# Kernel tuning notes

Measured on AMD Instinct MI355X. Metric: run time of the kernel, lower is better.

The kernel has to match this reference:

```python
import jax, jax.numpy as jnp
import numpy as np

B, Q, T, C = 2, 300, 25, 256
NH, NL, NP = 8, 4, 4
DFF = 1024
HD = C // NH
SHAPES = [(128, 128), (64, 64), (32, 32), (16, 16)]  # (H_l, W_l) per level
S = sum(h * w for h, w in SHAPES)
LQ = Q * T


def setup_inputs() -> dict:
    key = jax.random.key(0)
    ks = jax.random.split(key, 16)
    rn = lambda k, shape, s=0.02: jax.random.normal(k, shape, jnp.float32) * s
    starts = np.cumsum([0] + [h * w for h, w in SHAPES[:-1]])
    return {
        "tgt_text": jax.random.normal(ks[0], (B, Q, T, C), jnp.float32),
        "query_pos_text": jax.random.normal(ks[1], (B, Q, T, C), jnp.float32),
        "reference_points": jax.random.uniform(ks[2], (B, LQ, NL, 2), jnp.float32),
        "src": jax.random.normal(ks[3], (B, S, C), jnp.float32),
        "src_spatial_shapes": jnp.array(SHAPES, jnp.int32),
        "level_start_index": jnp.array(starts, jnp.int32),
        "in_proj_w": rn(ks[4], (3 * C, C)), "in_proj_b": jnp.zeros((3 * C,), jnp.float32),
        "out_proj_w": rn(ks[5], (C, C)), "out_proj_b": jnp.zeros((C,), jnp.float32),
        "ln1_g": jnp.ones((C,), jnp.float32), "ln1_b": jnp.zeros((C,), jnp.float32),
        "samp_off_w": rn(ks[6], (NH * NL * NP * 2, C)), "samp_off_b": rn(ks[7], (NH * NL * NP * 2,), 0.5),
        "aw_w": rn(ks[8], (NH * NL * NP, C)), "aw_b": jnp.zeros((NH * NL * NP,), jnp.float32),
        "vp_w": rn(ks[9], (C, C)), "vp_b": jnp.zeros((C,), jnp.float32),
        "op_w": rn(ks[10], (C, C)), "op_b": jnp.zeros((C,), jnp.float32),
        "ln2_g": jnp.ones((C,), jnp.float32), "ln2_b": jnp.zeros((C,), jnp.float32),
        "ffn1_w": rn(ks[11], (DFF, C)), "ffn1_b": jnp.zeros((DFF,), jnp.float32),
        "ffn2_w": rn(ks[12], (C, DFF)), "ffn2_b": jnp.zeros((C,), jnp.float32),
        "ln3_g": jnp.ones((C,), jnp.float32), "ln3_b": jnp.zeros((C,), jnp.float32),
    }


def _ln(x, g, b):
    m = jnp.mean(x, axis=-1, keepdims=True)
    v = jnp.var(x, axis=-1, keepdims=True)
    return (x - m) / jnp.sqrt(v + 1e-5) * g + b


def _self_attn(tgt, pos, in_proj_w, in_proj_b, out_proj_w, out_proj_b):
    # torch nn.MultiheadAttention math: q,k carry pos, v is raw tgt
    qk = (tgt + pos).reshape(B * Q, T, C)
    x = tgt.reshape(B * Q, T, C)
    Wq, Wk, Wv = jnp.split(in_proj_w, 3, axis=0)
    bq, bk, bv = jnp.split(in_proj_b, 3, axis=0)
    heads = lambda t: t.reshape(B * Q, T, NH, HD).transpose(0, 2, 1, 3)
    q = heads(qk @ Wq.T + bq)
    k = heads(qk @ Wk.T + bk)
    v = heads(x @ Wv.T + bv)
    attn = jax.nn.softmax(jnp.einsum("bhqd,bhkd->bhqk", q, k) / jnp.sqrt(jnp.float32(HD)), axis=-1)
    o = jnp.einsum("bhqk,bhkd->bhqd", attn, v).transpose(0, 2, 1, 3).reshape(B * Q, T, C)
    return (o @ out_proj_w.T + out_proj_b).reshape(B, Q, T, C)


def _ms_deform_attn(query, reference_points, src, shapes, samp_off_w, samp_off_b, aw_w, aw_b, vp_w, vp_b, op_w, op_b):
    # query: [B, LQ, C]; src: [B, S, C]
    value = (src @ vp_w.T + vp_b).reshape(B, S, NH, HD)
    off = (query @ samp_off_w.T + samp_off_b).reshape(B, LQ, NH, NL, NP, 2)
    aw = jax.nn.softmax((query @ aw_w.T + aw_b).reshape(B, LQ, NH, NL * NP), axis=-1)
    aw = aw.reshape(B, LQ, NH, NL, NP)
    # normalizer is (W_l, H_l)
    norm = jnp.array([[w, h] for (h, w) in shapes], jnp.float32)
    loc = reference_points[:, :, None, :, None, :] + off / norm[None, None, None, :, None, :]
    starts = np.cumsum([0] + [h * w for h, w in shapes])
    accum = jnp.zeros((B, NH, LQ, HD), jnp.float32)
    for l, (Hl, Wl) in enumerate(shapes):
        vl = value[:, starts[l]:starts[l] + Hl * Wl].transpose(0, 2, 1, 3)  # [B,NH,HW,HD]
        # grid_sample align_corners=False pixel coords
        xl = (loc[:, :, :, l, :, 0] * Wl - 0.5).transpose(0, 2, 1, 3).reshape(B, NH, LQ * NP)
        yl = (loc[:, :, :, l, :, 1] * Hl - 0.5).transpose(0, 2, 1, 3).reshape(B, NH, LQ * NP)
        x0 = jnp.floor(xl); y0 = jnp.floor(yl)
        wx1 = xl - x0; wy1 = yl - y0
        x0i = x0.astype(jnp.int32); y0i = y0.astype(jnp.int32)
        samp = jnp.zeros((B, NH, LQ * NP, HD), jnp.float32)
        for dx, dy, w in ((0, 0, (1 - wx1) * (1 - wy1)), (1, 0, wx1 * (1 - wy1)),
                          (0, 1, (1 - wx1) * wy1), (1, 1, wx1 * wy1)):
            xi = x0i + dx; yi = y0i + dy
            valid = (xi >= 0) & (xi < Wl) & (yi >= 0) & (yi < Hl)
            lin = jnp.clip(yi, 0, Hl - 1) * Wl + jnp.clip(xi, 0, Wl - 1)
            g = jnp.take_along_axis(vl, lin[..., None], axis=2)  # [B,NH,LQ*NP,HD]
            samp = samp + g * (w * valid)[..., None]
        samp = samp.reshape(B, NH, LQ, NP, HD)
        awl = aw[:, :, :, l, :].transpose(0, 2, 1, 3)  # [B,NH,LQ,NP]
        accum = accum + jnp.sum(samp * awl[..., None], axis=3)
    out = accum.transpose(0, 2, 1, 3).reshape(B, LQ, C)
    return out @ op_w.T + op_b


def reference(tgt_text, query_pos_text, reference_points, src, src_spatial_shapes, level_start_index,
              in_proj_w, in_proj_b, out_proj_w, out_proj_b, ln1_g, ln1_b,
              samp_off_w, samp_off_b, aw_w, aw_b, vp_w, vp_b, op_w, op_b, ln2_g, ln2_b,
              ffn1_w, ffn1_b, ffn2_w, ffn2_b, ln3_g, ln3_b):
    shapes = [tuple(int(v) for v in row) for row in np.asarray(src_spatial_shapes)]  # static
    # --- intra-text self-attention ---
    tgt2 = _self_attn(tgt_text, query_pos_text, in_proj_w, in_proj_b, out_proj_w, out_proj_b)
    tgt = _ln(tgt_text + tgt2, ln1_g, ln1_b)
    # --- multi-scale deformable cross-attention ---
    query = (tgt + query_pos_text).reshape(B, LQ, C)
    cross = _ms_deform_attn(query, reference_points, src, shapes,
                            samp_off_w, samp_off_b, aw_w, aw_b, vp_w, vp_b, op_w, op_b)
    tgt = _ln(tgt + cross.reshape(B, Q, T, C), ln2_g, ln2_b)
    # --- FFN ---
    ffn = jax.nn.relu(tgt @ ffn1_w.T + ffn1_b) @ ffn2_w.T + ffn2_b
    return _ln(tgt + ffn, ln3_g, ln3_b)
```

## Files before the change

kernel.cpp:

```cpp
#include <hip/hip_runtime.h>
#include <cstddef>

#define B_ 2
#define Q_ 300
#define T_ 25
#define C_ 256
#define NH_ 8
#define NL_ 4
#define NP_ 4
#define HD_ 32
#define DFF_ 1024
#define LQ_ (Q_ * T_)
#define NTOK_ (B_ * LQ_)
#define S_ 21760
#define BS_ (B_ * S_)

typedef __bf16 bf16x8 __attribute__((ext_vector_type(8)));
typedef float floatx4 __attribute__((ext_vector_type(4)));
typedef unsigned short ushort_t;

__device__ __forceinline__ unsigned pack_bf16(float x, float y) {
    unsigned ux = __float_as_uint(x) + 0x8000u;
    unsigned uy = __float_as_uint(y) + 0x8000u;
    return (ux >> 16) | (uy & 0xFFFF0000u);
}
__device__ __forceinline__ ushort_t f2bf_s(float x) {
    return (ushort_t)((__float_as_uint(x) + 0x8000u) >> 16);
}
__device__ __forceinline__ float bf2f(ushort_t u) {
    return __uint_as_float((unsigned)u << 16);
}

#define WOFF_IP   0
#define WOFF_OUT  196608
#define WOFF_VP   262144
#define WOFF_SO   327680
#define WOFF_AW   393216
#define WOFF_OP   425984
#define WOFF_F1   491520
#define WOFF_F2   753664
#define WTOTAL    1015808

__global__ __launch_bounds__(256) void convw_kernel(
    const float* __restrict__ ipw, const float* __restrict__ outw,
    const float* __restrict__ vpw, const float* __restrict__ sampw,
    const float* __restrict__ aww, const float* __restrict__ opw,
    const float* __restrict__ f1w, const float* __restrict__ f2w,
    ushort_t* __restrict__ dst)
{
    long long g = ((long long)blockIdx.x * 256 + threadIdx.x) * 8;
    if (g >= WTOTAL) return;
    const float* src; long long off;
    if      (g < WOFF_OUT) { src = ipw;   off = WOFF_IP; }
    else if (g < WOFF_VP)  { src = outw;  off = WOFF_OUT; }
    else if (g < WOFF_SO)  { src = vpw;   off = WOFF_VP; }
    else if (g < WOFF_AW)  { src = sampw; off = WOFF_SO; }
    else if (g < WOFF_OP)  { src = aww;   off = WOFF_AW; }
    else if (g < WOFF_F1)  { src = opw;   off = WOFF_OP; }
    else if (g < WOFF_F2)  { src = f1w;   off = WOFF_F1; }
    else                   { src = f2w;   off = WOFF_F2; }
    const float4* s4 = (const float4*)(src + (g - off));
    float4 a = s4[0], b = s4[1];
    uint4 o;
    o.x = pack_bf16(a.x, a.y); o.y = pack_bf16(a.z, a.w);
    o.z = pack_bf16(b.x, b.y); o.w = pack_bf16(b.z, b.w);
    *(uint4*)(dst + g) = o;
}

#define GBN 128
#define GBK 64
#define LDA_S 72

template<int AMODE, int OUTMODE, int GBMT>
__global__ __launch_bounds__(256) void gemm_w(
    const void* __restrict__ Av, const float* __restrict__ A2,
    const ushort_t* __restrict__ W,
    const float* __restrict__ bias, const float* __restrict__ bias2, int N1,
    void* __restrict__ Cv, long long partStride,
    int M, int N, int K, int kChunk, int ldc, int relu)
{
    constexpr int LA = GBMT / 16;
    constexpr int LB = 8;
    constexpr int WM = GBMT / 2;
    constexpr int NI = WM / 16;

    __shared__ unsigned short SH[GBMT * LDA_S + GBN * LDA_S];
    unsigned short* Asl = SH;
    unsigned short* Bsl = SH + GBMT * LDA_S;

    const int m0 = blockIdx.x * GBMT;
    if (m0 >= M) return;
    const int n0 = blockIdx.y * GBN;
    const int z  = blockIdx.z;
    const int kbeg = z * kChunk;
    const int kend = min(K, kbeg + kChunk);

    const int t  = threadIdx.x;
    const int wid  = t >> 6;
    const int lane = t & 63;
    const int wm = (wid >> 1) * WM;
    const int wn = (wid & 1) * 64;
    const int fm = lane & 15;
    const int fq = (lane >> 4) * 8;

    const bool addA2 = (AMODE == 1) && (n0 < N1);

    floatx4 acc[NI][4];
    #pragma unroll
    for (int i = 0; i < NI; ++i)
        #pragma unroll
        for (int j = 0; j < 4; ++j)
            acc[i][j] = (floatx4){0.f, 0.f, 0.f, 0.f};

    float4 pa[LA];
    uint2  pab[LA];
    uint2  pwb[LB];
    const float* Af = (const float*)Av;
    const ushort_t* Ab = (const ushort_t*)Av;

    auto load_tiles = [&](int k0) {
        #pragma unroll
        for (int i = 0; i < LA; ++i) {
            int idx = t + 256 * i;
            int row = idx >> 4;
            int c4  = (idx & 15) * 4;
            int gm = m0 + row;
            if constexpr (AMODE == 2) {
                uint2 v = {0u, 0u};
                if (gm < M) v = *(const uint2*)(Ab + (size_t)gm * K + k0 + c4);
                pab[i] = v;
            } else {
                float4 v = make_float4(0.f, 0.f, 0.f, 0.f);
                if (gm < M) {
                    v = *(const float4*)(Af + (size_t)gm * K + k0 + c4);
                    if constexpr (AMODE == 1) {
                        if (addA2) {
                            float4 v2 = *(const float4*)(A2 + (size_t)gm * K + k0 + c4);
                            v.x += v2.x; v.y += v2.y; v.z += v2.z; v.w += v2.w;
                        }
                    }
                }
                pa[i] = v;
            }
        }
        #pragma unroll
        for (int i = 0; i < LB; ++i) {
            int idx = t + 256 * i;
            int row = idx >> 4;
            int c4  = (idx & 15) * 4;
            pwb[i] = *(const uint2*)(W + (size_t)(n0 + row) * K + k0 + c4);
        }
    };

    load_tiles(kbeg);
    for (int k0 = kbeg; k0 < kend; k0 += GBK) {
        #pragma unroll
        for (int i = 0; i < LA; ++i) {
            int idx = t + 256 * i;
            int row = idx >> 4;
            int c4  = (idx & 15) * 4;
            if constexpr (AMODE == 2) {
                *(uint2*)&Asl[row * LDA_S + c4] = pab[i];
            } else {
                uint2 p;
                p.x = pack_bf16(pa[i].x, pa[i].y);
                p.y = pack_bf16(pa[i].z, pa[i].w);
                *(uint2*)&Asl[row * LDA_S + c4] = p;
            }
        }
        #pragma unroll
        for (int i = 0; i < LB; ++i) {
            int idx = t + 256 * i;
            int row = idx >> 4;
            int c4  = (idx & 15) * 4;
            *(uint2*)&Bsl[row * LDA_S + c4] = pwb[i];
        }
        __syncthreads();
        if (k0 + GBK < kend) load_tiles(k0 + GBK);

        #pragma unroll
        for (int kk = 0; kk < 2; ++kk) {
            bf16x8 af[NI], bfr[4];
            #pragma unroll
            for (int i = 0; i < NI; ++i)
                af[i] = *(const bf16x8*)&Asl[(wm + i * 16 + fm) * LDA_S + kk * 32 + fq];
            #pragma unroll
            for (int j = 0; j < 4; ++j)
                bfr[j] = *(const bf16x8*)&Bsl[(wn + j * 16 + fm) * LDA_S + kk * 32 + fq];

            #pragma unroll
            for (int i = 0; i < NI; ++i)
                #pragma unroll
                for (int j = 0; j < 4; ++j)
                    acc[i][j] = __builtin_amdgcn_mfma_f32_16x16x32_bf16(af[i], bfr[j], acc[i][j], 0, 0, 0);
        }
        __syncthreads();
    }

    float* Cf = (float*)Cv + (long long)z * partStride;
    ushort_t* Cb = (ushort_t*)Cv;
    const int cr = (lane >> 4) * 4;
    const int cc = lane & 15;

    if constexpr (OUTMODE == 0) {
        #pragma unroll
        for (int j = 0; j < 4; ++j) {
            int gn = n0 + wn + j * 16 + cc;
            float bia = 0.f;
            if (z == 0) bia = (bias2 && gn >= N1) ? bias2[gn - N1] : bias[gn];
            #pragma unroll
            for (int i = 0; i < NI; ++i)
                #pragma unroll
                for (int r = 0; r < 4; ++r) {
                    int gm = m0 + wm + i * 16 + cr + r;
                    if (gm < M) {
                        float v = acc[i][j][r] + bia;
                        if (relu) v = fmaxf(v, 0.f);
                        Cf[(size_t)gm * ldc + gn] = v;
                    }
                }
        }
    } else {
        unsigned short* epi = SH + wid * (WM * 64);
        #pragma unroll
        for (int j = 0; j < 4; ++j) {
            int gn = n0 + wn + j * 16 + cc;
            float bia = (bias2 && gn >= N1) ? bias2[gn - N1] : bias[gn];
            #pragma unroll
            for (int i = 0; i < NI; ++i)
                #pragma unroll
                for (int r = 0; r < 4; ++r) {
                    float v = acc[i][j][r] + bia;
                    if (relu) v = fmaxf(v, 0.f);
                    epi[(i * 16 + cr + r) * 64 + j * 16 + cc] = f2bf_s(v);
                }
        }
        #pragma unroll
        for (int pass = 0; pass < WM / 8; ++pass) {
            int lr = pass * 8 + (lane >> 3);
            int gm = m0 + wm + lr;
            uint4 vv = *(const uint4*)&epi[lr * 64 + (lane & 7) * 8];
            if (gm < M) {
                if constexpr (OUTMODE == 1) {
                    *(uint4*)&Cb[(size_t)gm * ldc + n0 + wn + (lane & 7) * 8] = vv;
                } else {
                    int bb = gm >= S_;
                    int s  = gm - bb * S_;
                    int gh = n0 + wn + (lane & 7) * 8;
                    *(uint4*)&Cb[(((size_t)(bb * 8 + (gh >> 5))) * S_ + s) * 32 + (gh & 31)] = vv;
                }
            }
        }
    }
}

__global__ __launch_bounds__(64) void attn_kernel(
    const ushort_t* __restrict__ qkv,
    ushort_t* __restrict__ o)
{
    int sh = blockIdx.x;
    int s = sh >> 3, h = sh & 7;
    __shared__ float qs[T_][HD_], ks[T_][HD_], vs[T_][HD_];
    int t = threadIdx.x;

    for (int idx = t; idx < T_ * HD_; idx += 64) {
        int i = idx >> 5, d = idx & 31;
        size_t base = ((size_t)(s * T_ + i)) * 768 + h * HD_ + d;
        qs[i][d] = bf2f(qkv[base]);
        ks[i][d] = bf2f(qkv[base + 256]);
        vs[i][d] = bf2f(qkv[base + 512]);
    }
    __syncthreads();

    if (t < T_) {
        float sc[T_];
        float mx = -1e30f;
        #pragma unroll
        for (int j = 0; j < T_; ++j) {
            float dot = 0.f;
            #pragma unroll
            for (int d = 0; d < HD_; ++d) dot += qs[t][d] * ks[j][d];
            sc[j] = dot * 0.17677669529663687f;
            mx = fmaxf(mx, sc[j]);
        }
        float sum = 0.f;
        #pragma unroll
        for (int j = 0; j < T_; ++j) { sc[j] = __expf(sc[j] - mx); sum += sc[j]; }
        float inv = 1.f / sum;
        float out[HD_];
        #pragma unroll
        for (int d = 0; d < HD_; ++d) out[d] = 0.f;
        for (int j = 0; j < T_; ++j) {
            float p = sc[j] * inv;
            #pragma unroll
            for (int d = 0; d < HD_; ++d) out[d] += p * vs[j][d];
        }
        size_t ob = ((size_t)(s * T_ + t)) * C_ + h * HD_;
        #pragma unroll
        for (int d = 0; d < HD_; ++d) o[ob + d] = f2bf_s(out[d]);
    }
}

__global__ __launch_bounds__(256) void ln4_kernel(
    const float* x, const float* r,
    int nparts, long long rstride,
    const float* __restrict__ g, const float* __restrict__ b,
    float* out, const float* __restrict__ pos,
    float* qout)
{
    const int wave = threadIdx.x >> 6;
    const int lane = threadIdx.x & 63;
    const int tok = blockIdx.x * 4 + wave;
    const size_t base = (size_t)tok * C_ + lane * 4;

    float4 v = *(const float4*)(x + base);
    for (int p = 0; p < nparts; ++p) {
        float4 rv = *(const float4*)(r + base + (long long)p * rstride);
        v.x += rv.x; v.y += rv.y; v.z += rv.z; v.w += rv.w;
    }
    float s  = v.x + v.y + v.z + v.w;
    float ss = v.x * v.x + v.y * v.y + v.z * v.z + v.w * v.w;
    #pragma unroll
    for (int m = 32; m; m >>= 1) {
        s  += __shfl_xor(s, m);
        ss += __shfl_xor(ss, m);
    }
    float mean = s * (1.f / 256.f);
    float var  = ss * (1.f / 256.f) - mean * mean;
    float rstd = rsqrtf(var + 1e-5f);

    float4 gv = *(const float4*)(g + lane * 4);
    float4 bv = *(const float4*)(b + lane * 4);
    float4 y;
    y.x = (v.x - mean) * rstd * gv.x + bv.x;
    y.y = (v.y - mean) * rstd * gv.y + bv.y;
    y.z = (v.z - mean) * rstd * gv.z + bv.z;
    y.w = (v.w - mean) * rstd * gv.w + bv.w;
    *(float4*)(out + base) = y;
    if (qout) {
        float4 pv = *(const float4*)(pos + base);
        float4 q;
        q.x = y.x + pv.x; q.y = y.y + pv.y; q.z = y.z + pv.z; q.w = y.w + pv.w;
        *(float4*)(qout + base) = q;
    }
}

#define DCHUNK_ 118
__global__ __launch_bounds__(256, 4) void deform_kernel(
    const ushort_t* __restrict__ value,
    const float* __restrict__ d12,
    const float* __restrict__ refpts,
    ushort_t* __restrict__ out)
{
    const int bi    = blockIdx.x;
    const int xcd   = bi & 7;
    const int yy    = bi >> 3;
    const int combo = xcd + 8 * (yy & 1);
    const int chunk = yy >> 1;
    const int h     = combo & 7;
    const int b     = combo >> 3;

    __shared__ float tls[64][60];

    const int tid = threadIdx.x;
    const int t0  = chunk * 64;

    #pragma unroll
    for (int i = 0; i < 2; ++i) {
        int idx  = tid + 256 * i;
        int trw  = idx >> 3;
        int c4   = (idx & 7) * 4;
        int tl   = min(t0 + trw, LQ_ - 1);
        float4 v;
        v.x = __builtin_nontemporal_load(d12 + (size_t)(b * LQ_ + tl) * 384 + h * 32 + c4 + 0);
        v.y = __builtin_nontemporal_load(d12 + (size_t)(b * LQ_ + tl) * 384 + h * 32 + c4 + 1);
        v.z = __builtin_nontemporal_load(d12 + (size_t)(b * LQ_ + tl) * 384 + h * 32 + c4 + 2);
        v.w = __builtin_nontemporal_load(d12 + (size_t)(b * LQ_ + tl) * 384 + h * 32 + c4 + 3);
        *(float4*)&tls[trw][c4] = v;
    }
    {
        int trw = tid >> 2;
        int c4  = (tid & 3) * 4;
        int tl  = min(t0 + trw, LQ_ - 1);
        float4 v;
        v.x = __builtin_nontemporal_load(d12 + (size_t)(b * LQ_ + tl) * 384 + 256 + h * 16 + c4 + 0);
        v.y = __builtin_nontemporal_load(d12 + (size_t)(b * LQ_ + tl) * 384 + 256 + h * 16 + c4 + 1);
        v.z = __builtin_nontemporal_load(d12 + (size_t)(b * LQ_ + tl) * 384 + 256 + h * 16 + c4 + 2);
        v.w = __builtin_nontemporal_load(d12 + (size_t)(b * LQ_ + tl) * 384 + 256 + h * 16 + c4 + 3);
        *(float4*)&tls[trw][32 + c4] = v;
    }
    if (tid < 128) {
        int trw = tid >> 1;
        int c4  = (tid & 1) * 4;
        int tl  = min(t0 + trw, LQ_ - 1);
        float4 v;
        v.x = __builtin_nontemporal_load(refpts + (size_t)(b * LQ_ + tl) * 8 + c4 + 0);
        v.y = __builtin_nontemporal_load(refpts + (size_t)(b * LQ_ + tl) * 8 + c4 + 1);
        v.z = __builtin_nontemporal_load(refpts + (size_t)(b * LQ_ + tl) * 8 + c4 + 2);
        v.w = __builtin_nontemporal_load(refpts + (size_t)(b * LQ_ + tl) * 8 + c4 + 3);
        *(float4*)&tls[trw][48 + c4] = v;
    }
    __syncthreads();

    if (tid < 64) {
        float lg[16];
        float mx = -1e30f;
        #pragma unroll
        for (int i = 0; i < 16; ++i) { lg[i] = tls[tid][32 + i]; mx = fmaxf(mx, lg[i]); }
        float sum = 0.f;
        #pragma unroll
        for (int i = 0; i < 16; ++i) { lg[i] = __expf(lg[i] - mx); sum += lg[i]; }
        float inv = 1.f / sum;
        #pragma unroll
        for (int i = 0; i < 16; ++i) tls[tid][32 + i] = lg[i] * inv;
    }
    __syncthreads();

    const int wave = tid >> 6;
    const int lane = tid & 63;
    const int ti   = lane >> 2;
    const int d8   = (lane & 3) * 8;
    const int row  = wave * 16 + ti;

    int tl = t0 + row;
    const bool active = (tl < LQ_);
    tl = min(tl, LQ_ - 1);
    const int tok = b * LQ_ + tl;

    const int HW[4]     = {128, 64, 32, 16};
    const int starts[4] = {0, 16384, 20480, 21504};

    const ushort_t* vplane = value + (size_t)combo * ((size_t)S_ * HD_) + d8;
    const float* trow = tls[row];

    float accv[8];
    #pragma unroll
    for (int i = 0; i < 8; ++i) accv[i] = 0.f;

    #pragma unroll
    for (int l = 0; l < 4; ++l) {
        const int Hl = HW[l], Wl = HW[l];
        float rx = trow[48 + l * 2 + 0];
        float ry = trow[48 + l * 2 + 1];
        const ushort_t* vbase = vplane + (size_t)starts[l] * HD_;

        int   voff[16];
        float wgt[16];
        #pragma unroll
        for (int p = 0; p < 4; ++p) {
            float ox = trow[l * 8 + p * 2 + 0];
            float oy = trow[l * 8 + p * 2 + 1];
            float aww = trow[32 + l * 4 + p];
            float xl = rx * (float)Wl + ox - 0.5f;
            float yl = ry * (float)Hl + oy - 0.5f;
            float x0f = floorf(xl), y0f = floorf(yl);
            int x0 = (int)x0f, y0 = (int)y0f;
            float wx1 = xl - x0f, wy1 = yl - y0f;
            float wx0 = 1.f - wx1, wy0 = 1.f - wy1;
            #pragma unroll
            for (int c = 0; c < 4; ++c) {
                int dx = c & 1, dy = c >> 1;
                int xi = x0 + dx, yi = y0 + dy;
                float w = (dx ? wx1 : wx0) * (dy ? wy1 : wy0);
                bool valid = (xi >= 0) & (xi < Wl) & (yi >= 0) & (yi < Hl);
                int xc = min(max(xi, 0), Wl - 1);
                int yc = min(max(yi, 0), Hl - 1);
                voff[p * 4 + c] = yc * Wl + xc;
                wgt[p * 4 + c]  = (valid ? w : 0.f) * aww;
            }
        }
        uint4 raw[16];
        #pragma unroll
        for (int i = 0; i < 16; ++i)
            raw[i] = *(const uint4*)(vbase + (size_t)voff[i] * HD_);
        #pragma unroll
        for (int i = 0; i < 16; ++i) {
            float wc = wgt[i];
            accv[0] += __uint_as_float((raw[i].x & 0xFFFFu) << 16) * wc;
            accv[1] += __uint_as_float(raw[i].x & 0xFFFF0000u) * wc;
            accv[2] += __uint_as_float((raw[i].y & 0xFFFFu) << 16) * wc;
            accv[3] += __uint_as_float(raw[i].y & 0xFFFF0000u) * wc;
            accv[4] += __uint_as_float((raw[i].z & 0xFFFFu) << 16) * wc;
            accv[5] += __uint_as_float(raw[i].z & 0xFFFF0000u) * wc;
            accv[6] += __uint_as_float((raw[i].w & 0xFFFFu) << 16) * wc;
            accv[7] += __uint_as_float(raw[i].w & 0xFFFF0000u) * wc;
        }
    }
    if (active) {
        uint4 po;
        po.x = pack_bf16(accv[0], accv[1]);
        po.y = pack_bf16(accv[2], accv[3]);
        po.z = pack_bf16(accv[4], accv[5]);
        po.w = pack_bf16(accv[6], accv[7]);
        *(uint4*)(out + (size_t)tok * C_ + h * HD_ + d8) = po;
    }
}

extern "C" void kernel_launch(void* const* d_in, const int* in_sizes, int n_in,
                              void* d_out, int out_size, void* d_ws, size_t ws_size,
                              hipStream_t stream) {
    const float* tgt_text = (const float*)d_in[0];
    const float* pos      = (const float*)d_in[1];
    const float* refpts   = (const float*)d_in[2];
    const float* src      = (const float*)d_in[3];
    const float* in_proj_w  = (const float*)d_in[6];
    const float* in_proj_b  = (const float*)d_in[7];
    const float* out_proj_w = (const float*)d_in[8];
    const float* out_proj_b = (const float*)d_in[9];
    const float* ln1_g = (const float*)d_in[10];
    const float* ln1_b = (const float*)d_in[11];
    const float* samp_off_w = (const float*)d_in[12];
    const float* samp_off_b = (const float*)d_in[13];
    const float* aw_w = (const float*)d_in[14];
    const float* aw_b = (const float*)d_in[15];
    const float* vp_w = (const float*)d_in[16];
    const float* vp_b = (const float*)d_in[17];
    const float* op_w = (const float*)d_in[18];
    const float* op_b = (const float*)d_in[19];
    const float* ln2_g = (const float*)d_in[20];
    const float* ln2_b = (const float*)d_in[21];
    const float* ffn1_w = (const float*)d_in[22];
    const float* ffn1_b = (const float*)d_in[23];
    const float* ffn2_w = (const float*)d_in[24];
    const float* ffn2_b = (const float*)d_in[25];
    const float* ln3_g = (const float*)d_in[26];
    const float* ln3_b = (const float*)d_in[27];

    const long long NC = (long long)NTOK_ * C_;
    float* ws = (float*)d_ws;
    float* A    = ws;
    float* Bq   = ws + NC;
    float* Creg = ws + 2 * NC;
    float* D12  = Creg + (long long)NTOK_ * DFF_;
    float* E    = D12 + (long long)NTOK_ * 384;
    float* F    = E + NC;
    ushort_t* wb = (ushort_t*)(F + NC);

    ushort_t* qkv  = (ushort_t*)Creg;
    ushort_t* valt = (ushort_t*)Creg + (size_t)NTOK_ * 768;

    const int MB64P  = 240;
    const int MB128P = 120;
    const int MBV64  = BS_ / 64;

    convw_kernel<<<496, 256, 0, stream>>>(in_proj_w, out_proj_w, vp_w, samp_off_w,
                                          aw_w, op_w, ffn1_w, ffn2_w, wb);
    gemm_w<1, 1, 64><<<dim3(MB64P, 6, 1), 256, 0, stream>>>(tgt_text, pos, wb + WOFF_IP,
        in_proj_b, nullptr, 512, qkv, 0, NTOK_, 768, 256, 256, 768, 0);
    gemm_w<0, 2, 64><<<dim3(MBV64, 2, 1), 256, 0, stream>>>(src, nullptr, wb + WOFF_VP,
        vp_b, nullptr, 0, valt, 0, BS_, 256, 256, 256, 0, 0);
    attn_kernel<<<B_ * Q_ * NH_, 64, 0, stream>>>(qkv, (ushort_t*)E);
    gemm_w<2, 0, 64><<<dim3(MB64P, 2, 1), 256, 0, stream>>>(E, nullptr, wb + WOFF_OUT,
        out_proj_b, nullptr, 0, F, 0, NTOK_, 256, 256, 256, 256, 0);
    ln4_kernel<<<NTOK_ / 4, 256, 0, stream>>>(tgt_text, F, 1, 0,
                                              ln1_g, ln1_b, A, pos, Bq);
    gemm_w<0, 0, 64><<<dim3(MB64P, 3, 1), 256, 0, stream>>>(Bq, nullptr, wb + WOFF_SO,
        samp_off_b, aw_b, 256, D12, 0, NTOK_, 384, 256, 256, 384, 0);
    deform_kernel<<<8 * 2 * DCHUNK_, 256, 0, stream>>>(valt, D12, refpts, (ushort_t*)E);
    gemm_w<2, 0, 64><<<dim3(MB64P, 2, 1), 256, 0, stream>>>(E, nullptr, wb + WOFF_OP,
        op_b, nullptr, 0, F, 0, NTOK_, 256, 256, 256, 256, 0);
    ln4_kernel<<<NTOK_ / 4, 256, 0, stream>>>(A, F, 1, 0,
                                              ln2_g, ln2_b, A, nullptr, nullptr);
    gemm_w<0, 1, 128><<<dim3(MB128P, 8, 1), 256, 0, stream>>>(A, nullptr, wb + WOFF_F1,
        ffn1_b, nullptr, 0, Creg, 0, NTOK_, DFF_, 256, 256, DFF_, 1);
    gemm_w<2, 0, 128><<<dim3(MB128P, 2, 2), 256, 0, stream>>>(Creg, nullptr, wb + WOFF_F2,
        ffn2_b, nullptr, 0, E, NC, NTOK_, 256, 1024, 512, 256, 0);
    ln4_kernel<<<NTOK_ / 4, 256, 0, stream>>>(A, E, 2, NC,
                                              ln3_g, ln3_b, (float*)d_out, nullptr, nullptr);
}
```

Before: 384.2 us.

## Fuse N=256 output GEMMs with residual add and LayerNorm in one kernel

Adds a gemm_ln kernel that computes a full 64x256 output row tile per block (bf16 MFMA), then applies bias, residual add and LayerNorm in the epilogue, optionally writing the pos-added query. It replaces the out_proj, deformable output proj and FFN2 GEMMs plus their separate ln4 kernels, removing the fp32 intermediate write and re-read and three launches. The FFN2 split-K over two partial buffers is dropped, so each of 240 blocks now runs the full K=1024 alone, which lowers parallelism and may lengthen that GEMM.

```diff
diff --git a/kernel.cpp b/kernel.cpp
--- a/kernel.cpp
+++ b/kernel.cpp
@@ -254,6 +254,144 @@
     }
 }
 
+template<int KSTEPS>
+__global__ __launch_bounds__(256) void gemm_ln(
+    const ushort_t* __restrict__ Ab,
+    const ushort_t* __restrict__ W,
+    const float* __restrict__ bias,
+    const float* x,
+    const float* __restrict__ g, const float* __restrict__ bv_,
+    const float* __restrict__ pos,
+    float* outp, float* qout, int M)
+{
+    constexpr int K = KSTEPS * 64;
+    __shared__ unsigned short SH[(64 + 256) * LDA_S];
+    unsigned short* Asl = SH;
+    unsigned short* Bsl = SH + 64 * LDA_S;
+
+    const int m0 = blockIdx.x * 64;
+    if (m0 >= M) return;
+
+    const int t    = threadIdx.x;
+    const int wid  = t >> 6;
+    const int lane = t & 63;
+    const int wm   = wid * 16;
+    const int fm   = lane & 15;
+    const int fq   = (lane >> 4) * 8;
+
+    floatx4 acc[16];
+    #pragma unroll
+    for (int j = 0; j < 16; ++j) acc[j] = (floatx4){0.f, 0.f, 0.f, 0.f};
+
+    uint2 pab[4];
+    uint2 pwb[16];
+
+    auto load_tiles = [&](int k0) {
+        #pragma unroll
+        for (int i = 0; i < 4; ++i) {
+            int idx = t + 256 * i;
+            int row = idx >> 4;
+            int c4  = (idx & 15) * 4;
+            int gm  = m0 + row;
+            uint2 v = {0u, 0u};
+            if (gm < M) v = *(const uint2*)(Ab + (size_t)gm * K + k0 + c4);
+            pab[i] = v;
+        }
+        #pragma unroll
+        for (int i = 0; i < 16; ++i) {
+            int idx = t + 256 * i;
+            int row = idx >> 4;
+            int c4  = (idx & 15) * 4;
+            pwb[i] = *(const uint2*)(W + (size_t)row * K + k0 + c4);
+        }
+    };
+
+    load_tiles(0);
+    #pragma unroll 1
+    for (int ks = 0; ks < KSTEPS; ++ks) {
+        #pragma unroll
+        for (int i = 0; i < 4; ++i) {
+            int idx = t + 256 * i;
+            *(uint2*)&Asl[(idx >> 4) * LDA_S + (idx & 15) * 4] = pab[i];
+        }
+        #pragma unroll
+        for (int i = 0; i < 16; ++i) {
+            int idx = t + 256 * i;
+            *(uint2*)&Bsl[(idx >> 4) * LDA_S + (idx & 15) * 4] = pwb[i];
+        }
+        __syncthreads();
+        if (ks + 1 < KSTEPS) load_tiles((ks + 1) * 64);
+
+        #pragma unroll
+        for (int kk = 0; kk < 2; ++kk) {
+            bf16x8 af = *(const bf16x8*)&Asl[(wm + fm) * LDA_S + kk * 32 + fq];
+            #pragma unroll
+            for (int j = 0; j < 16; ++j) {
+                bf16x8 bfr = *(const bf16x8*)&Bsl[(j * 16 + fm) * LDA_S + kk * 32 + fq];
+                acc[j] = __builtin_amdgcn_mfma_f32_16x16x32_bf16(af, bfr, acc[j], 0, 0, 0);
+            }
+        }
+        __syncthreads();
+    }
+
+    const int cr = (lane >> 4) * 4;
+    const int cc = lane & 15;
+    float* ep = (float*)SH;
+    float4 gv = *(const float4*)(g   + lane * 4);
+    float4 bb = *(const float4*)(bv_ + lane * 4);
+
+    #pragma unroll
+    for (int half = 0; half < 2; ++half) {
+        if ((wid >> 1) == half) {
+            int rbase = wm & 31;
+            #pragma unroll
+            for (int j = 0; j < 16; ++j) {
+                float bia = bias[j * 16 + cc];
+                #pragma unroll
+                for (int r = 0; r < 4; ++r)
+                    ep[(rbase + cr + r) * 264 + j * 16 + cc] = acc[j][r] + bia;
+            }
+        }
+        __syncthreads();
+
+        #pragma unroll
+        for (int pass = 0; pass < 8; ++pass) {
+            int rl   = pass * 4 + wid;
+            int grow = m0 + half * 32 + rl;
+            float4 v = *(const float4*)&ep[rl * 264 + lane * 4];
+            if (grow < M) {
+                float4 xv = *(const float4*)(x + (size_t)grow * 256 + lane * 4);
+                v.x += xv.x; v.y += xv.y; v.z += xv.z; v.w += xv.w;
+            }
+            float s  = v.x + v.y + v.z + v.w;
+            float ss = v.x * v.x + v.y * v.y + v.z * v.z + v.w * v.w;
+            #pragma unroll
+            for (int m = 32; m; m >>= 1) {
+                s  += __shfl_xor(s, m);
+                ss += __shfl_xor(ss, m);
+            }
+            float mean = s * (1.f / 256.f);
+            float var  = ss * (1.f / 256.f) - mean * mean;
+            float rstd = rsqrtf(var + 1e-5f);
+            float4 y;
+            y.x = (v.x - mean) * rstd * gv.x + bb.x;
+            y.y = (v.y - mean) * rstd * gv.y + bb.y;
+            y.z = (v.z - mean) * rstd * gv.z + bb.z;
+            y.w = (v.w - mean) * rstd * gv.w + bb.w;
+            if (grow < M) {
+                *(float4*)(outp + (size_t)grow * 256 + lane * 4) = y;
+                if (qout) {
+                    float4 pv = *(const float4*)(pos + (size_t)grow * 256 + lane * 4);
+                    float4 q;
+                    q.x = y.x + pv.x; q.y = y.y + pv.y; q.z = y.z + pv.z; q.w = y.w + pv.w;
+                    *(float4*)(qout + (size_t)grow * 256 + lane * 4) = q;
+                }
+            }
+        }
+        __syncthreads();
+    }
+}
+
 __global__ __launch_bounds__(64) void attn_kernel(
     const ushort_t* __restrict__ qkv,
     ushort_t* __restrict__ o)
@@ -298,50 +436,6 @@
         size_t ob = ((size_t)(s * T_ + t)) * C_ + h * HD_;
         #pragma unroll
         for (int d = 0; d < HD_; ++d) o[ob + d] = f2bf_s(out[d]);
-    }
-}
-
-__global__ __launch_bounds__(256) void ln4_kernel(
-    const float* x, const float* r,
-    int nparts, long long rstride,
-    const float* __restrict__ g, const float* __restrict__ b,
-    float* out, const float* __restrict__ pos,
-    float* qout)
-{
-    const int wave = threadIdx.x >> 6;
-    const int lane = threadIdx.x & 63;
-    const int tok = blockIdx.x * 4 + wave;
-    const size_t base = (size_t)tok * C_ + lane * 4;
-
-    float4 v = *(const float4*)(x + base);
-    for (int p = 0; p < nparts; ++p) {
-        float4 rv = *(const float4*)(r + base + (long long)p * rstride);
-        v.x += rv.x; v.y += rv.y; v.z += rv.z; v.w += rv.w;
-    }
-    float s  = v.x + v.y + v.z + v.w;
-    float ss = v.x * v.x + v.y * v.y + v.z * v.z + v.w * v.w;
-    #pragma unroll
-    for (int m = 32; m; m >>= 1) {
-        s  += __shfl_xor(s, m);
-        ss += __shfl_xor(ss, m);
-    }
-    float mean = s * (1.f / 256.f);
-    float var  = ss * (1.f / 256.f) - mean * mean;
-    float rstd = rsqrtf(var + 1e-5f);
-
-    float4 gv = *(const float4*)(g + lane * 4);
-    float4 bv = *(const float4*)(b + lane * 4);
-    float4 y;
-    y.x = (v.x - mean) * rstd * gv.x + bv.x;
-    y.y = (v.y - mean) * rstd * gv.y + bv.y;
-    y.z = (v.z - mean) * rstd * gv.z + bv.z;
-    y.w = (v.w - mean) * rstd * gv.w + bv.w;
-    *(float4*)(out + base) = y;
-    if (qout) {
-        float4 pv = *(const float4*)(pos + base);
-        float4 q;
-        q.x = y.x + pv.x; q.y = y.y + pv.y; q.z = y.z + pv.z; q.w = y.w + pv.w;
-        *(float4*)(qout + base) = q;
     }
 }
 
@@ -550,21 +644,15 @@
     gemm_w<0, 2, 64><<<dim3(MBV64, 2, 1), 256, 0, stream>>>(src, nullptr, wb + WOFF_VP,
         vp_b, nullptr, 0, valt, 0, BS_, 256, 256, 256, 0, 0);
     attn_kernel<<<B_ * Q_ * NH_, 64, 0, stream>>>(qkv, (ushort_t*)E);
-    gemm_w<2, 0, 64><<<dim3(MB64P, 2, 1), 256, 0, stream>>>(E, nullptr, wb + WOFF_OUT,
-        out_proj_b, nullptr, 0, F, 0, NTOK_, 256, 256, 256, 256, 0);
-    ln4_kernel<<<NTOK_ / 4, 256, 0, stream>>>(tgt_text, F, 1, 0,
-                                              ln1_g, ln1_b, A, pos, Bq);
+    gemm_ln<4><<<MB64P, 256, 0, stream>>>((ushort_t*)E, wb + WOFF_OUT, out_proj_b,
+        tgt_text, ln1_g, ln1_b, pos, A, Bq, NTOK_);
     gemm_w<0, 0, 64><<<dim3(MB64P, 3, 1), 256, 0, stream>>>(Bq, nullptr, wb + WOFF_SO,
         samp_off_b, aw_b, 256, D12, 0, NTOK_, 384, 256, 256, 384, 0);
     deform_kernel<<<8 * 2 * DCHUNK_, 256, 0, stream>>>(valt, D12, refpts, (ushort_t*)E);
-    gemm_w<2, 0, 64><<<dim3(MB64P, 2, 1), 256, 0, stream>>>(E, nullptr, wb + WOFF_OP,
-        op_b, nullptr, 0, F, 0, NTOK_, 256, 256, 256, 256, 0);
-    ln4_kernel<<<NTOK_ / 4, 256, 0, stream>>>(A, F, 1, 0,
-                                              ln2_g, ln2_b, A, nullptr, nullptr);
+    gemm_ln<4><<<MB64P, 256, 0, stream>>>((ushort_t*)E, wb + WOFF_OP, op_b,
+        A, ln2_g, ln2_b, nullptr, A, nullptr, NTOK_);
     gemm_w<0, 1, 128><<<dim3(MB128P, 8, 1), 256, 0, stream>>>(A, nullptr, wb + WOFF_F1,
         ffn1_b, nullptr, 0, Creg, 0, NTOK_, DFF_, 256, 256, DFF_, 1);
-    gemm_w<2, 0, 128><<<dim3(MB128P, 2, 2), 256, 0, stream>>>(Creg, nullptr, wb + WOFF_F2,
-        ffn2_b, nullptr, 0, E, NC, NTOK_, 256, 1024, 512, 256, 0);
-    ln4_kernel<<<NTOK_ / 4, 256, 0, stream>>>(A, E, 2, NC,
-                                              ln3_g, ln3_b, (float*)d_out, nullptr, nullptr);
-}
+    gemm_ln<16><<<MB64P, 256, 0, stream>>>((ushort_t*)Creg, wb + WOFF_F2, ffn2_b,
+        A, ln3_g, ln3_b, nullptr, (float*)d_out, nullptr, NTOK_);
+}
```

Result: no change. 377.2 us (-1.8%).
